# Kernel tuning notes

Hardware: AMD Instinct MI355X
Metric: run time of the kernel (lower is better)

## Reference

```python
import jax, jax.numpy as jnp
import numpy as np

N = 50000          # number of rows / ego agents
A = 65             # num_agents + 1 (slot dimension)
DEG = 32           # neighbors per row
EMB = 32           # embedding_dim
HID = 16           # mlp hidden (mlp_pre_pool_dims = [32, 16, 32])
BOT = 32           # bottleneck_dim = h_dim
NEG_INF = -jnp.inf


def setup_inputs() -> dict:
    key = jax.random.key(0)
    ks = jax.random.split(key, 8)
    corr_index = jax.random.normal(ks[0], (N, A, 2), dtype=jnp.float32)
    lstm_state = jax.random.normal(ks[1], (N, BOT), dtype=jnp.float32)
    # edge list with unique (row, slot) pairs so scatter-set is well defined
    col0 = np.repeat(np.arange(N, dtype=np.int32), DEG)
    col2 = np.tile(np.arange(DEG, dtype=np.int32), N)
    col1 = np.random.default_rng(1).integers(0, A, size=N * DEG).astype(np.int32)
    nei_index = jnp.asarray(np.stack([col0, col1, col2], axis=1))  # [E,3]
    # parameters (Linear weights stored as [in, out])
    def lin(k, fin, fout):
        bound = 1.0 / np.sqrt(fin)
        kw, kb = jax.random.split(k)
        W = jax.random.uniform(kw, (fin, fout), jnp.float32, -bound, bound)
        b = jax.random.uniform(kb, (fout,), jnp.float32, -bound, bound)
        return W, b
    W_se, b_se = lin(ks[2], 2, EMB)
    W1, b1 = lin(ks[3], EMB, HID)
    W2, b2 = lin(ks[4], HID, BOT)
    return {"corr_index": corr_index, "nei_index": nei_index,
            "lstm_state": lstm_state, "W_se": W_se, "b_se": b_se,
            "W1": W1, "b1": b1, "W2": W2, "b2": b2}


def reference(corr_index, nei_index, lstm_state, W_se, b_se, W1, b1, W2, b2):
    # gather relative positions for each edge: [E, 2]
    rel = corr_index[nei_index[:, 0], nei_index[:, 1]]
    # spatial embedding + MLP (Linear+ReLU, Linear+ReLU)
    r_t = rel @ W_se + b_se                         # [E, EMB]
    h = jax.nn.relu(r_t @ W1 + b1)                  # [E, HID]
    h = jax.nn.relu(h @ W2 + b2)                    # [E, BOT]
    # scatter into dense -inf buffer, max over slot dim, zero out empty rows
    H = jnp.full((N, A, BOT), NEG_INF, dtype=h.dtype)
    H = H.at[nei_index[:, 0], nei_index[:, 2]].set(h, unique_indices=True)
    pool_h = jnp.max(H, axis=1)                     # [N, BOT]
    pool_h = jnp.where(jnp.isneginf(pool_h), 0.0, pool_h)
    return pool_h
```

## Files before the change

### kernel.cpp

```cpp
#include <hip/hip_runtime.h>
#include <hip/hip_bf16.h>

#define NODES 50000
#define NA    65
#define NDEG  32


typedef float v2f __attribute__((ext_vector_type(2)));
typedef __attribute__((ext_vector_type(8))) short short8;
typedef __attribute__((ext_vector_type(16))) float f32x16;

static __device__ __forceinline__ v2f pk_fma(v2f a, v2f b, v2f c) {
    return __builtin_elementwise_fma(a, b, c);
}
static __device__ __forceinline__ v2f pk_max(v2f a, v2f b) {
    return __builtin_elementwise_max(a, b);
}

__global__ __launch_bounds__(256, 1) void fused_kernel(
    const float* __restrict__ corr,
    const int*   __restrict__ nei,
    const float* __restrict__ W_se,
    const float* __restrict__ b_se,
    const float* __restrict__ W1,
    const float* __restrict__ b1,
    const float* __restrict__ W2,
    const float* __restrict__ b2,
    float* __restrict__ out)
{
    __shared__ __align__(16) float  fold[48];
    __shared__ __align__(16) float2 relbuf[32 * 32];

    int t  = threadIdx.x;
    int nb = blockIdx.x * 32;

    if (t < 48) {
        float s;
        if (t < 32) {
            int c = t >> 4, j = t & 15;
            s = 0.0f;
#pragma unroll
            for (int e = 0; e < 32; ++e)
                s = fmaf(W_se[c * 32 + e], W1[e * 16 + j], s);
        } else {
            int j = t - 32;
            s = b1[j];
#pragma unroll
            for (int e = 0; e < 32; ++e)
                s = fmaf(b_se[e], W1[e * 16 + j], s);
        }
        fold[t] = s;
    }

#pragma unroll
    for (int u = 0; u < 4; ++u) {
        int g    = t + 256 * u;
        int nl   = g >> 5;
        int d    = g & 31;
        int node = nb + nl;
        if (node < NODES) {
            int idx = nei[((size_t)node * NDEG + d) * 3 + 1];
            relbuf[nl * 32 + d] = ((const float2*)corr)[(size_t)node * NA + idx];
        }
    }
    __syncthreads();

    int lane  = t & 63;
    int w     = t >> 6;
    int col   = lane & 31;
    int khalf = lane >> 5;

    v2f wc0v[4], wc1v[4], bcv[4];
    {
        const float* fb = fold + khalf * 8;
#pragma unroll
        for (int p = 0; p < 4; ++p) {
            wc0v[p] = *(const v2f*)(fb + 2 * p);
            wc1v[p] = *(const v2f*)(fb + 16 + 2 * p);
            bcv[p]  = *(const v2f*)(fb + 32 + 2 * p);
        }
    }

    union FragU { short8 s8; __hip_bfloat162 h2[4]; };
    FragU bu;
#pragma unroll
    for (int p = 0; p < 4; ++p) {
        int k = khalf * 8 + 2 * p;
        bu.h2[p] = __float22bfloat162_rn(
            make_float2(W2[k * 32 + col], W2[(k + 1) * 32 + col]));
    }
    float b2c = b2[col];

    f32x16 czero;
#pragma unroll
    for (int j = 0; j < 16; ++j) czero[j] = 0.0f;

    const float2* rp = relbuf + w * 8 * 32;

#pragma unroll
    for (int i = 0; i < 8; ++i) {
        int node = nb + w * 8 + i;
        if (node >= NODES) break;

        float2 r = rp[i * 32 + col];
        v2f r0s = {r.x, r.x}, r1s = {r.y, r.y};

        FragU au;
#pragma unroll
        for (int p = 0; p < 4; ++p) {
            v2f h = pk_max((v2f)(0.0f),
                     pk_fma(r0s, wc0v[p], pk_fma(r1s, wc1v[p], bcv[p])));
            au.h2[p] = __float22bfloat162_rn(make_float2(h.x, h.y));
        }

        f32x16 acc = __builtin_amdgcn_mfma_f32_32x32x16_bf16(au.s8, bu.s8, czero, 0, 0, 0);

        float m = acc[0];
#pragma unroll
        for (int j = 1; j < 16; ++j) m = fmaxf(m, acc[j]);
        m = fmaxf(m, __shfl_xor(m, 32, 64));

        float res = fmaxf(0.0f, m + b2c);
        if (lane < 32) out[(size_t)node * 32 + col] = res;
    }
}

extern "C" void kernel_launch(void* const* d_in, const int* in_sizes, int n_in,
                              void* d_out, int out_size, void* d_ws, size_t ws_size,
                              hipStream_t stream) {
    const float* corr = (const float*)d_in[0];
    const int*   nei  = (const int*)d_in[1];
    const float* W_se = (const float*)d_in[3];
    const float* b_se = (const float*)d_in[4];
    const float* W1   = (const float*)d_in[5];
    const float* b1   = (const float*)d_in[6];
    const float* W2   = (const float*)d_in[7];
    const float* b2   = (const float*)d_in[8];
    float* out = (float*)d_out;

    int blocks = (NODES + 31) / 32;
    hipLaunchKernelGGL(fused_kernel, dim3(blocks), dim3(256), 0, stream,
                       corr, nei, W_se, b_se, W1, b1, W2, b2, out);
}
```

Measured before the change: 105.0 us.

## Gather relative positions directly into registers and tree-reduce MFMA outputs

Each lane now loads its own neighbor indices and corr values for its 8 nodes straight into registers, replacing the shared-memory relbuf staging. All global loads, including W2 and b2, are issued before the barrier so they overlap the weight-folding step. Out-of-range nodes are clamped instead of exiting the loop early. The 16-element max reduction uses a packed pairwise tree instead of a serial chain. This costs more registers, and both lane halves now redundantly load the same indices and positions.

```diff
diff --git a/kernel.cpp b/kernel.cpp
--- a/kernel.cpp
+++ b/kernel.cpp
@@ -28,11 +28,21 @@
     const float* __restrict__ b2,
     float* __restrict__ out)
 {
-    __shared__ __align__(16) float  fold[48];
-    __shared__ __align__(16) float2 relbuf[32 * 32];
+    __shared__ __align__(16) float fold[48];
 
-    int t  = threadIdx.x;
-    int nb = blockIdx.x * 32;
+    int t     = threadIdx.x;
+    int lane  = t & 63;
+    int w     = t >> 6;
+    int col   = lane & 31;
+    int khalf = lane >> 5;
+    int nbase = blockIdx.x * 32 + w * 8;
+
+    int idxv[8];
+#pragma unroll
+    for (int i = 0; i < 8; ++i) {
+        int node = nbase + i; if (node > NODES - 1) node = NODES - 1;
+        idxv[i] = nei[((size_t)node * NDEG + col) * 3 + 1];
+    }
 
     if (t < 48) {
         float s;
@@ -52,23 +62,24 @@
         fold[t] = s;
     }
 
+    float2 rel[8];
 #pragma unroll
-    for (int u = 0; u < 4; ++u) {
-        int g    = t + 256 * u;
-        int nl   = g >> 5;
-        int d    = g & 31;
-        int node = nb + nl;
-        if (node < NODES) {
-            int idx = nei[((size_t)node * NDEG + d) * 3 + 1];
-            relbuf[nl * 32 + d] = ((const float2*)corr)[(size_t)node * NA + idx];
-        }
+    for (int i = 0; i < 8; ++i) {
+        int node = nbase + i; if (node > NODES - 1) node = NODES - 1;
+        rel[i] = ((const float2*)corr)[(size_t)node * NA + idxv[i]];
     }
+
+    union FragU { short8 s8; __hip_bfloat162 h2[4]; };
+    FragU bu;
+#pragma unroll
+    for (int p = 0; p < 4; ++p) {
+        int k = khalf * 8 + 2 * p;
+        bu.h2[p] = __float22bfloat162_rn(
+            make_float2(W2[k * 32 + col], W2[(k + 1) * 32 + col]));
+    }
+    float b2c = b2[col];
+
     __syncthreads();
-
-    int lane  = t & 63;
-    int w     = t >> 6;
-    int col   = lane & 31;
-    int khalf = lane >> 5;
 
     v2f wc0v[4], wc1v[4], bcv[4];
     {
@@ -81,29 +92,15 @@
         }
     }
 
-    union FragU { short8 s8; __hip_bfloat162 h2[4]; };
-    FragU bu;
-#pragma unroll
-    for (int p = 0; p < 4; ++p) {
-        int k = khalf * 8 + 2 * p;
-        bu.h2[p] = __float22bfloat162_rn(
-            make_float2(W2[k * 32 + col], W2[(k + 1) * 32 + col]));
-    }
-    float b2c = b2[col];
-
     f32x16 czero;
 #pragma unroll
     for (int j = 0; j < 16; ++j) czero[j] = 0.0f;
 
-    const float2* rp = relbuf + w * 8 * 32;
-
 #pragma unroll
     for (int i = 0; i < 8; ++i) {
-        int node = nb + w * 8 + i;
-        if (node >= NODES) break;
+        int node = nbase + i;
 
-        float2 r = rp[i * 32 + col];
-        v2f r0s = {r.x, r.x}, r1s = {r.y, r.y};
+        v2f r0s = {rel[i].x, rel[i].x}, r1s = {rel[i].y, rel[i].y};
 
         FragU au;
 #pragma unroll
@@ -115,13 +112,19 @@
 
         f32x16 acc = __builtin_amdgcn_mfma_f32_32x32x16_bf16(au.s8, bu.s8, czero, 0, 0, 0);
 
-        float m = acc[0];
-#pragma unroll
-        for (int j = 1; j < 16; ++j) m = fmaxf(m, acc[j]);
+        v2f p0 = pk_max((v2f){acc[0],  acc[1]},  (v2f){acc[2],  acc[3]});
+        v2f p1 = pk_max((v2f){acc[4],  acc[5]},  (v2f){acc[6],  acc[7]});
+        v2f p2 = pk_max((v2f){acc[8],  acc[9]},  (v2f){acc[10], acc[11]});
+        v2f p3 = pk_max((v2f){acc[12], acc[13]}, (v2f){acc[14], acc[15]});
+        v2f q0 = pk_max(p0, p1);
+        v2f q1 = pk_max(p2, p3);
+        v2f rr = pk_max(q0, q1);
+        float m = fmaxf(rr.x, rr.y);
         m = fmaxf(m, __shfl_xor(m, 32, 64));
 
         float res = fmaxf(0.0f, m + b2c);
-        if (lane < 32) out[(size_t)node * 32 + col] = res;
+        if (lane < 32 && node < NODES)
+            out[(size_t)node * 32 + col] = res;
     }
 }
 
```

New measurement: 104.0 us, median of 2. Within noise of the previous version (-0.9%).
